# Optimization experiments

Hardware: AMD Instinct MI355X
Metric: run time of the kernel (lower is better)

## Reference

```python
import jax, jax.numpy as jnp
import numpy as np

B, S, V, F = 8, 500, 100, 5          # batch, n_samples(=500 hard-coded), n_vertices, n_feat
NT, NR = 4, 3                         # n_thetas, n_rhos
K = NT * NR                           # gaussian kernels = 12
MAX_RHO = 12.0
N_ROT = 1
EPS = 1e-5
TWO_PI = 2.0 * np.pi


def _initial_coords():
    # faithful to compute_initial_coordinates(): rho-major flattening
    grid_rho = np.linspace(0.0, MAX_RHO, NR + 1)[1:]
    grid_theta = np.linspace(0.0, TWO_PI, NT + 1)[:-1]
    r_, t_ = np.meshgrid(grid_rho, grid_theta)
    return r_.T.flatten().astype(np.float32), t_.T.flatten().astype(np.float32)


def setup_inputs() -> dict:
    key = jax.random.key(0)
    ks = jax.random.split(key, 8)
    input_feat = jax.random.normal(ks[0], (B, S, V, F), jnp.float32)
    rho_coords = jax.random.uniform(ks[1], (B, S, V, 1), jnp.float32) * MAX_RHO
    theta_coords = jax.random.uniform(ks[2], (B, S, V, 1), jnp.float32) * TWO_PI
    mask = (jax.random.uniform(ks[3], (B, S, V, 1)) > 0.1).astype(jnp.float32)
    mr, mt = _initial_coords()
    mu_rho = jnp.tile(jnp.asarray(mr)[None, :], (F, 1))          # [F,K]
    mu_theta = jnp.tile(jnp.asarray(mt)[None, :], (F, 1))        # [F,K]
    sigma_rho = jnp.full((F, K), MAX_RHO / 8.0, jnp.float32)
    sigma_theta = jnp.ones((F, K), jnp.float32)
    W_conv = jax.random.normal(ks[4], (F, K, K), jnp.float32) * (1.0 / np.sqrt(K))
    b_conv = jnp.zeros((F, K), jnp.float32)
    W2 = jax.random.normal(ks[5], (F * K, K), jnp.float32) * (1.0 / np.sqrt(F * K))
    b2 = jnp.zeros((K,), jnp.float32)
    W3 = jax.random.normal(ks[6], (K, F), jnp.float32) * (1.0 / np.sqrt(K))
    b3 = jnp.zeros((F,), jnp.float32)
    W4 = jax.random.normal(ks[7], (F, 3), jnp.float32) * (1.0 / np.sqrt(F))
    b4 = jnp.zeros((3,), jnp.float32)
    return dict(input_feat=input_feat, rho_coords=rho_coords, theta_coords=theta_coords,
                mask=mask, mu_rho=mu_rho, sigma_rho=sigma_rho, mu_theta=mu_theta,
                sigma_theta=sigma_theta, W_conv=W_conv, b_conv=b_conv,
                W2=W2, b2=b2, W3=W3, b3=b3, W4=W4, b4=b4)


def reference(input_feat, rho_coords, theta_coords, mask, mu_rho, sigma_rho,
              mu_theta, sigma_theta, W_conv, b_conv, W2, b2, W3, b3, W4, b4):
    rho = rho_coords[..., 0]    # [B,S,V]
    th0 = theta_coords[..., 0]  # [B,S,V]
    # Gaussian in rho, per feature channel f and kernel k -> [B,F,S,V,K]
    g_rho = jnp.exp(-(rho[:, None, :, :, None] - mu_rho[None, :, None, None, :]) ** 2
                    / (sigma_rho[None, :, None, None, :] ** 2 + EPS))
    m = mask[:, None, :, :, :]  # [B,1,S,V,1]
    convs = []
    for r in range(N_ROT):
        th = jnp.mod(th0 + r * TWO_PI / N_ROT, TWO_PI)
        g_th = jnp.exp(-(th[:, None, :, :, None] - mu_theta[None, :, None, None, :]) ** 2
                       / (sigma_theta[None, :, None, None, :] ** 2 + EPS))
        g = g_rho * g_th * m                                   # [B,F,S,V,K]
        # NOTE: source normalizes over axis 1 (the n_samples/patch axis), faithful here (axis=2 in BFSVK)
        g = g / (jnp.sum(g, axis=2, keepdims=True) + EPS)
        desc = jnp.einsum('bfsvk,bsvf->bfsk', g, input_feat)   # sum over vertices
        convs.append(jnp.einsum('bfsk,fkj->bfsj', desc, W_conv) + b_conv[None, :, None, :])
    conv = jax.nn.relu(jnp.max(jnp.stack(convs, 0), 0))        # [B,F,S,K]
    gd = conv.transpose(0, 2, 1, 3).reshape(B, S, F * K)       # stack axis=2 order (F then K)
    h = jax.nn.relu(gd @ W2 + b2)
    h = jax.nn.relu(h @ W3 + b3)
    return jax.nn.softmax(h @ W4 + b4, axis=-1)                # [B,S,3]
```

## Files before the change

### kernel.cpp

```cpp
#include <hip/hip_runtime.h>
#include <math.h>

namespace {
constexpr int Bc = 8, Sc = 500, Vc = 100, Fc = 5, Kc = 12, FKc = 60;
constexpr int BV = Bc * Vc;
constexpr int NDEN = BV * FKc;
constexpr int VG = 25;
constexpr float EPSc = 1e-5f;
}

__device__ __forceinline__ void gauss_consts(
    const float* __restrict__ mu_rho, const float* __restrict__ sigma_rho,
    const float* __restrict__ mu_theta, const float* __restrict__ sigma_theta,
    int fk,
    float& nr1, float& nr2, float& nr3,
    float& nt1, float& nt2, float& nt3)
{
    float mr = mu_rho[fk],  sr = sigma_rho[fk];
    float mt = mu_theta[fk], st = sigma_theta[fk];
    float isr = 1.0f / (sr * sr + EPSc);
    float ist = 1.0f / (st * st + EPSc);
    nr1 = -isr; nr2 = 2.0f * isr * mr; nr3 = -(isr * mr) * mr;
    nt1 = -ist; nt2 = 2.0f * ist * mt; nt3 = -(ist * mt) * mt;
}

__global__ __launch_bounds__(64) void k_denom_partial(
    const float* __restrict__ rho, const float* __restrict__ theta,
    const float* __restrict__ mask,
    const float* __restrict__ mu_rho, const float* __restrict__ sigma_rho,
    const float* __restrict__ mu_theta, const float* __restrict__ sigma_theta,
    float* __restrict__ partial, int chunk)
{
    const int c  = blockIdx.x;
    const int b  = blockIdx.y;
    const int wg = blockIdx.z;
    const int lane = threadIdx.x;
    const int fk = lane < FKc ? lane : FKc - 1;
    const int v0 = wg * VG;

    float nr1, nr2, nr3, nt1, nt2, nt3;
    gauss_consts(mu_rho, sigma_rho, mu_theta, sigma_theta, fk,
                 nr1, nr2, nr3, nt1, nt2, nt3);

    const int s0 = c * chunk;
    const int s1 = min(Sc, s0 + chunk);

    float acc[VG];
#pragma unroll
    for (int i = 0; i < VG; ++i) acc[i] = 0.0f;

    const size_t base = (size_t)b * Sc * Vc + v0;
    for (int s = s0; s < s1; ++s) {
        const float* rp = rho   + base + (size_t)s * Vc;
        const float* tp = theta + base + (size_t)s * Vc;
        const float* mp = mask  + base + (size_t)s * Vc;
#pragma unroll
        for (int vi = 0; vi < VG; ++vi) {
            float r = rp[vi], t = tp[vi], m = mp[vi];
            float ar = __fmaf_rn(__fmaf_rn(nr1, r, nr2), r, nr3);
            float at = __fmaf_rn(__fmaf_rn(nt1, t, nt2), t, nt3 + ar);
            acc[vi] = __fmaf_rn(__expf(at), m, acc[vi]);
        }
    }

    float* pp = partial + (size_t)c * NDEN + ((size_t)b * Vc + v0) * FKc;
    if (lane < FKc) {
#pragma unroll
        for (int vi = 0; vi < VG; ++vi)
            pp[(size_t)vi * FKc + lane] = acc[vi];
    }
}

__global__ __launch_bounds__(256) void k_inv(
    const float* __restrict__ partial, float* __restrict__ inv_denom, int SCH)
{
    const int i = blockIdx.x * 256 + threadIdx.x;
    if (i >= NDEN) return;
    float s = 0.0f;
#pragma unroll 4
    for (int c = 0; c < SCH; ++c)
        s += partial[(size_t)c * NDEN + i];
    inv_denom[i] = 1.0f / (s + EPSc);
}

__global__ __launch_bounds__(64) void k_main(
    const float* __restrict__ feat, const float* __restrict__ rho,
    const float* __restrict__ theta, const float* __restrict__ mask,
    const float* __restrict__ mu_rho, const float* __restrict__ sigma_rho,
    const float* __restrict__ mu_theta, const float* __restrict__ sigma_theta,
    const float* __restrict__ Wc, const float* __restrict__ bc,
    const float* __restrict__ W2, const float* __restrict__ b2,
    const float* __restrict__ W3, const float* __restrict__ b3,
    const float* __restrict__ W4, const float* __restrict__ b4,
    const float* __restrict__ inv_denom,
    float* __restrict__ out)
{
    const int bs = blockIdx.x;
    const int b = bs / Sc;
    const int lane = threadIdx.x;
    const int fk = lane < FKc ? lane : FKc - 1;
    const int f = fk / Kc;

    __shared__ float lds_feat[Vc * Fc];
    __shared__ float lds_r[Vc];
    __shared__ float lds_t[Vc];
    __shared__ float lds_m[Vc];
    __shared__ float lds_wc[Fc * Kc * Kc];
    __shared__ float lds_w2[FKc * Kc];
    __shared__ float lds_desc[FKc];
    __shared__ float lds_gd[FKc];
    __shared__ float lds_h1[Kc];
    __shared__ float lds_h2[Fc];
    __shared__ float lds_logit[3];

    {
        const float4* s_f = (const float4*)(feat + (size_t)bs * Vc * Fc);
        float4* d_f = (float4*)lds_feat;
#pragma unroll
        for (int i = lane; i < Vc * Fc / 4; i += 64) d_f[i] = s_f[i];

        const float4* s_r = (const float4*)(rho   + (size_t)bs * Vc);
        const float4* s_t = (const float4*)(theta + (size_t)bs * Vc);
        const float4* s_m = (const float4*)(mask  + (size_t)bs * Vc);
        if (lane < Vc / 4) {
            ((float4*)lds_r)[lane] = s_r[lane];
            ((float4*)lds_t)[lane] = s_t[lane];
            ((float4*)lds_m)[lane] = s_m[lane];
        }
        const float4* s_wc = (const float4*)Wc;
        const float4* s_w2 = (const float4*)W2;
        float4* d_wc = (float4*)lds_wc;
        float4* d_w2 = (float4*)lds_w2;
#pragma unroll
        for (int i = lane; i < Fc * Kc * Kc / 4; i += 64) {
            d_wc[i] = s_wc[i];
            d_w2[i] = s_w2[i];
        }
    }

    float nr1, nr2, nr3, nt1, nt2, nt3;
    gauss_consts(mu_rho, sigma_rho, mu_theta, sigma_theta, fk,
                 nr1, nr2, nr3, nt1, nt2, nt3);

    __syncthreads();

    const size_t base_bv = (size_t)b * Vc;
    float acc = 0.0f;
#pragma unroll 10
    for (int v = 0; v < Vc; ++v) {
        float id = inv_denom[(base_bv + v) * FKc + fk];
        float r = lds_r[v];
        float t = lds_t[v];
        float m = lds_m[v];
        float fv = lds_feat[v * Fc + f];
        float ar = __fmaf_rn(__fmaf_rn(nr1, r, nr2), r, nr3);
        float at = __fmaf_rn(__fmaf_rn(nt1, t, nt2), t, nt3 + ar);
        acc = __fmaf_rn(__expf(at) * m * id, fv, acc);
    }
    if (lane < FKc) lds_desc[lane] = acc;
    __syncthreads();

    if (lane < FKc) {
        const int ff = lane / Kc, j = lane % Kc;
        float sum = bc[lane];
#pragma unroll
        for (int k = 0; k < Kc; ++k)
            sum = __fmaf_rn(lds_desc[ff * Kc + k],
                            lds_wc[ff * Kc * Kc + k * Kc + j], sum);
        lds_gd[lane] = fmaxf(sum, 0.0f);
    }
    __syncthreads();

    if (lane < Kc) {
        float sum = b2[lane];
#pragma unroll
        for (int i = 0; i < FKc; ++i)
            sum = __fmaf_rn(lds_gd[i], lds_w2[i * Kc + lane], sum);
        lds_h1[lane] = fmaxf(sum, 0.0f);
    }
    __syncthreads();

    if (lane < Fc) {
        float sum = b3[lane];
#pragma unroll
        for (int i = 0; i < Kc; ++i)
            sum = __fmaf_rn(lds_h1[i], W3[i * Fc + lane], sum);
        lds_h2[lane] = fmaxf(sum, 0.0f);
    }
    __syncthreads();

    if (lane < 3) {
        float sum = b4[lane];
#pragma unroll
        for (int i = 0; i < Fc; ++i)
            sum = __fmaf_rn(lds_h2[i], W4[i * 3 + lane], sum);
        lds_logit[lane] = sum;
    }
    __syncthreads();

    if (lane < 3) {
        float l0 = lds_logit[0], l1 = lds_logit[1], l2 = lds_logit[2];
        float mx = fmaxf(l0, fmaxf(l1, l2));
        float e0 = __expf(l0 - mx), e1 = __expf(l1 - mx), e2 = __expf(l2 - mx);
        float inv = 1.0f / (e0 + e1 + e2);
        float mine = lane == 0 ? e0 : (lane == 1 ? e1 : e2);
        out[(size_t)bs * 3 + lane] = mine * inv;
    }
}

extern "C" void kernel_launch(void* const* d_in, const int* in_sizes, int n_in,
                              void* d_out, int out_size, void* d_ws, size_t ws_size,
                              hipStream_t stream) {
    const float* feat     = (const float*)d_in[0];
    const float* rho      = (const float*)d_in[1];
    const float* theta    = (const float*)d_in[2];
    const float* mask     = (const float*)d_in[3];
    const float* mu_rho   = (const float*)d_in[4];
    const float* sig_rho  = (const float*)d_in[5];
    const float* mu_theta = (const float*)d_in[6];
    const float* sig_th   = (const float*)d_in[7];
    const float* Wc       = (const float*)d_in[8];
    const float* bc       = (const float*)d_in[9];
    const float* W2       = (const float*)d_in[10];
    const float* b2       = (const float*)d_in[11];
    const float* W3       = (const float*)d_in[12];
    const float* b3       = (const float*)d_in[13];
    const float* W4       = (const float*)d_in[14];
    const float* b4       = (const float*)d_in[15];

    float* inv_denom = (float*)d_ws;
    const size_t inv_bytes = (size_t)NDEN * 4;
    size_t rem = ws_size > inv_bytes ? ws_size - inv_bytes : 0;
    int SCH = (int)(rem / inv_bytes);
    if (SCH > 100) SCH = 100;
    float* partial;
    if (SCH < 1) { SCH = 1; partial = inv_denom; }
    else partial = inv_denom + NDEN;
    const int chunk = (Sc + SCH - 1) / SCH;

    k_denom_partial<<<dim3(SCH, Bc, 4), 64, 0, stream>>>(
        rho, theta, mask, mu_rho, sig_rho, mu_theta, sig_th, partial, chunk);

    k_inv<<<(NDEN + 255) / 256, 256, 0, stream>>>(partial, inv_denom, SCH);

    k_main<<<Bc * Sc, 64, 0, stream>>>(
        feat, rho, theta, mask, mu_rho, sig_rho, mu_theta, sig_th,
        Wc, bc, W2, b2, W3, b3, W4, b4, inv_denom, (float*)d_out);
}
```

Baseline: 126.8 us.

## Compute denominators per (b,v) block in one kernel, drop partial-sum pass

Replaces the chunked partial-denominator kernel and its separate reduction kernel with a single kernel that has one block per (batch, vertex). Two waves each sweep half of the samples, and the halves are combined through shared memory before the reciprocal is written. This removes a kernel launch and the partial-sum round trip through global memory. The main kernel also stops staging Wc and W2 in LDS and reads them from global memory through the cache. The new loads are strided by V across samples, so each block's inputs are gathered scalars rather than contiguous runs.

```diff
diff --git a/kernel.cpp b/kernel.cpp
--- a/kernel.cpp
+++ b/kernel.cpp
@@ -3,9 +3,6 @@
 
 namespace {
 constexpr int Bc = 8, Sc = 500, Vc = 100, Fc = 5, Kc = 12, FKc = 60;
-constexpr int BV = Bc * Vc;
-constexpr int NDEN = BV * FKc;
-constexpr int VG = 25;
 constexpr float EPSc = 1e-5f;
 }
 
@@ -24,63 +21,49 @@
     nt1 = -ist; nt2 = 2.0f * ist * mt; nt3 = -(ist * mt) * mt;
 }
 
-__global__ __launch_bounds__(64) void k_denom_partial(
+__global__ __launch_bounds__(128) void k_denom2(
     const float* __restrict__ rho, const float* __restrict__ theta,
     const float* __restrict__ mask,
     const float* __restrict__ mu_rho, const float* __restrict__ sigma_rho,
     const float* __restrict__ mu_theta, const float* __restrict__ sigma_theta,
-    float* __restrict__ partial, int chunk)
+    float* __restrict__ inv_denom)
 {
-    const int c  = blockIdx.x;
-    const int b  = blockIdx.y;
-    const int wg = blockIdx.z;
-    const int lane = threadIdx.x;
+    const int bv = blockIdx.x;
+    const int b = bv / Vc, v = bv % Vc;
+    const int w = threadIdx.x >> 6;
+    const int lane = threadIdx.x & 63;
     const int fk = lane < FKc ? lane : FKc - 1;
-    const int v0 = wg * VG;
 
     float nr1, nr2, nr3, nt1, nt2, nt3;
     gauss_consts(mu_rho, sigma_rho, mu_theta, sigma_theta, fk,
                  nr1, nr2, nr3, nt1, nt2, nt3);
 
-    const int s0 = c * chunk;
-    const int s1 = min(Sc, s0 + chunk);
-
-    float acc[VG];
-#pragma unroll
-    for (int i = 0; i < VG; ++i) acc[i] = 0.0f;
-
-    const size_t base = (size_t)b * Sc * Vc + v0;
-    for (int s = s0; s < s1; ++s) {
-        const float* rp = rho   + base + (size_t)s * Vc;
-        const float* tp = theta + base + (size_t)s * Vc;
-        const float* mp = mask  + base + (size_t)s * Vc;
-#pragma unroll
-        for (int vi = 0; vi < VG; ++vi) {
-            float r = rp[vi], t = tp[vi], m = mp[vi];
-            float ar = __fmaf_rn(__fmaf_rn(nr1, r, nr2), r, nr3);
-            float at = __fmaf_rn(__fmaf_rn(nt1, t, nt2), t, nt3 + ar);
-            acc[vi] = __fmaf_rn(__expf(at), m, acc[vi]);
+    const size_t base = (size_t)b * Sc * Vc + v;
+    const int s0 = w * (Sc / 2);
+
+    float a0 = 0.f, a1 = 0.f, a2 = 0.f, a3 = 0.f, a4 = 0.f;
+    for (int i = 0; i < Sc / 2; i += 5) {
+        const size_t p = base + (size_t)(s0 + i) * Vc;
+#define GSTEP(J, ACC)                                                        \
+        {                                                                    \
+            float r = rho[p + (size_t)(J) * Vc];                             \
+            float t = theta[p + (size_t)(J) * Vc];                           \
+            float m = mask[p + (size_t)(J) * Vc];                            \
+            float ar = __fmaf_rn(__fmaf_rn(nr1, r, nr2), r, nr3);            \
+            float at = __fmaf_rn(__fmaf_rn(nt1, t, nt2), t, nt3 + ar);       \
+            ACC = __fmaf_rn(__expf(at), m, ACC);                             \
         }
-    }
-
-    float* pp = partial + (size_t)c * NDEN + ((size_t)b * Vc + v0) * FKc;
-    if (lane < FKc) {
-#pragma unroll
-        for (int vi = 0; vi < VG; ++vi)
-            pp[(size_t)vi * FKc + lane] = acc[vi];
-    }
-}
-
-__global__ __launch_bounds__(256) void k_inv(
-    const float* __restrict__ partial, float* __restrict__ inv_denom, int SCH)
-{
-    const int i = blockIdx.x * 256 + threadIdx.x;
-    if (i >= NDEN) return;
-    float s = 0.0f;
-#pragma unroll 4
-    for (int c = 0; c < SCH; ++c)
-        s += partial[(size_t)c * NDEN + i];
-    inv_denom[i] = 1.0f / (s + EPSc);
+        GSTEP(0, a0) GSTEP(1, a1) GSTEP(2, a2) GSTEP(3, a3) GSTEP(4, a4)
+#undef GSTEP
+    }
+    float acc = ((a0 + a1) + (a2 + a3)) + a4;
+
+    __shared__ float red[2][64];
+    red[w][lane] = acc;
+    __syncthreads();
+    if (w == 0 && lane < FKc)
+        inv_denom[(size_t)bv * FKc + lane] =
+            1.0f / (red[0][lane] + red[1][lane] + EPSc);
 }
 
 __global__ __launch_bounds__(64) void k_main(
@@ -105,8 +88,6 @@
     __shared__ float lds_r[Vc];
     __shared__ float lds_t[Vc];
     __shared__ float lds_m[Vc];
-    __shared__ float lds_wc[Fc * Kc * Kc];
-    __shared__ float lds_w2[FKc * Kc];
     __shared__ float lds_desc[FKc];
     __shared__ float lds_gd[FKc];
     __shared__ float lds_h1[Kc];
@@ -126,15 +107,6 @@
             ((float4*)lds_r)[lane] = s_r[lane];
             ((float4*)lds_t)[lane] = s_t[lane];
             ((float4*)lds_m)[lane] = s_m[lane];
-        }
-        const float4* s_wc = (const float4*)Wc;
-        const float4* s_w2 = (const float4*)W2;
-        float4* d_wc = (float4*)lds_wc;
-        float4* d_w2 = (float4*)lds_w2;
-#pragma unroll
-        for (int i = lane; i < Fc * Kc * Kc / 4; i += 64) {
-            d_wc[i] = s_wc[i];
-            d_w2[i] = s_w2[i];
         }
     }
 
@@ -166,7 +138,7 @@
 #pragma unroll
         for (int k = 0; k < Kc; ++k)
             sum = __fmaf_rn(lds_desc[ff * Kc + k],
-                            lds_wc[ff * Kc * Kc + k * Kc + j], sum);
+                            Wc[ff * Kc * Kc + k * Kc + j], sum);
         lds_gd[lane] = fmaxf(sum, 0.0f);
     }
     __syncthreads();
@@ -175,7 +147,7 @@
         float sum = b2[lane];
 #pragma unroll
         for (int i = 0; i < FKc; ++i)
-            sum = __fmaf_rn(lds_gd[i], lds_w2[i * Kc + lane], sum);
+            sum = __fmaf_rn(lds_gd[i], W2[i * Kc + lane], sum);
         lds_h1[lane] = fmaxf(sum, 0.0f);
     }
     __syncthreads();
@@ -229,19 +201,9 @@
     const float* b4       = (const float*)d_in[15];
 
     float* inv_denom = (float*)d_ws;
-    const size_t inv_bytes = (size_t)NDEN * 4;
-    size_t rem = ws_size > inv_bytes ? ws_size - inv_bytes : 0;
-    int SCH = (int)(rem / inv_bytes);
-    if (SCH > 100) SCH = 100;
-    float* partial;
-    if (SCH < 1) { SCH = 1; partial = inv_denom; }
-    else partial = inv_denom + NDEN;
-    const int chunk = (Sc + SCH - 1) / SCH;
-
-    k_denom_partial<<<dim3(SCH, Bc, 4), 64, 0, stream>>>(
-        rho, theta, mask, mu_rho, sig_rho, mu_theta, sig_th, partial, chunk);
-
-    k_inv<<<(NDEN + 255) / 256, 256, 0, stream>>>(partial, inv_denom, SCH);
+
+    k_denom2<<<Bc * Vc, 128, 0, stream>>>(
+        rho, theta, mask, mu_rho, sig_rho, mu_theta, sig_th, inv_denom);
 
     k_main<<<Bc * Sc, 64, 0, stream>>>(
         feat, rho, theta, mask, mu_rho, sig_rho, mu_theta, sig_th,
```

Measured after the change: 124.0 us. 1.02x faster.
